# Kernel tuning notes

Measured on AMD Instinct MI355X. Metric: run time of the kernel, lower is better.

The kernel has to match this reference:

```python
import jax, jax.numpy as jnp
import numpy as np

B, N_PER, D = 128, 512, 128        # graphs, nodes per graph, feature width
N = B * N_PER                      # 65536 total nodes
E = 524288                         # total edges (avg degree 8)
KS = (410, 328, 263)               # ceil(0.8*512), ceil(0.8*410), ceil(0.8*328)


def setup_inputs() -> dict:
    key = jax.random.key(0)
    ks = jax.random.split(key, 20)
    p = lambda k, shape: jax.random.normal(k, shape, jnp.float32) * 0.05
    rng = np.random.default_rng(0)
    g = rng.integers(0, B, size=E)
    s = rng.integers(0, N_PER, size=E)
    t = rng.integers(0, N_PER, size=E)
    edge_index = jnp.asarray(np.stack([g * N_PER + s, g * N_PER + t]).astype(np.int32))
    inp = {
        'x': jax.random.normal(ks[0], (N, 1, D), jnp.float32),
        'edge_index': edge_index,
    }
    i = 1
    for l in (1, 2, 3):
        inp[f'conv{l}_wl'] = p(ks[i], (D, D)); i += 1   # SAGEConv lin_l (neighbors) weight
        inp[f'conv{l}_bl'] = p(ks[i], (D,));  i += 1   # SAGEConv lin_l bias
        inp[f'conv{l}_wr'] = p(ks[i], (D, D)); i += 1   # SAGEConv lin_r (root) weight
        inp[f'pool{l}_w'] = p(ks[i], (D,));   i += 1   # TopKPooling score vector
    inp['lin1_w'] = p(ks[13], (128, 256)); inp['lin1_b'] = p(ks[14], (128,))
    inp['lin2_w'] = p(ks[15], (64, 128));  inp['lin2_b'] = p(ks[16], (64,))
    inp['lin3_w'] = p(ks[17], (1, 64));    inp['lin3_b'] = p(ks[18], (1,))
    return inp


def _sage(x, node_mask, src, dst, wl, bl, wr):
    # SAGEConv, mean aggregation: lin_l(mean_{j->i} x_j) + lin_r(x_i)
    em = (node_mask[src] & node_mask[dst]).astype(x.dtype)   # [E] valid-edge mask
    msum = jax.ops.segment_sum(x[src] * em[:, None], dst, num_segments=N)
    deg = jax.ops.segment_sum(em, dst, num_segments=N)
    mean = msum / jnp.maximum(deg, 1.0)[:, None]
    return mean @ wl.T + bl + x @ wr.T


def _topk_pool(x, node_mask, w, k):
    # TopKPooling: score = x.w/||w||; keep top-k per graph; gate kept x by tanh(score)
    score = (x @ w) / (jnp.linalg.norm(w) + 1e-16)           # [N]
    score = jnp.where(node_mask, score, -jnp.inf)
    _, idx = jax.lax.top_k(score.reshape(B, N_PER), k)       # [B, k] within-graph ids
    nm = jnp.zeros((B, N_PER), bool).at[jnp.arange(B)[:, None], idx].set(True).reshape(-1)
    x = jnp.where(nm[:, None], x * jnp.tanh(score)[:, None], 0.0)
    return x, nm


def _readout(x, node_mask, k):
    # cat([global_max_pool, global_mean_pool]) over the k surviving nodes per graph
    xb = x.reshape(B, N_PER, -1)
    mb = node_mask.reshape(B, N_PER, 1)
    gmax = jnp.max(jnp.where(mb, xb, -jnp.inf), axis=1)
    gmean = jnp.sum(jnp.where(mb, xb, 0.0), axis=1) / k
    return jnp.concatenate([gmax, gmean], axis=1)            # [B, 2D]


def _forward(edge_index, x, conv1_wl, conv1_bl, conv1_wr, pool1_w,
             conv2_wl, conv2_bl, conv2_wr, pool2_w,
             conv3_wl, conv3_bl, conv3_wr, pool3_w,
             lin1_w, lin1_b, lin2_w, lin2_b, lin3_w, lin3_b):
    src, dst = edge_index[0], edge_index[1]
    h = x[:, 0, :]                                           # x.squeeze(1) -> [N, D]
    nm = jnp.ones((N,), bool)
    layers = ((conv1_wl, conv1_bl, conv1_wr, pool1_w),
              (conv2_wl, conv2_bl, conv2_wr, pool2_w),
              (conv3_wl, conv3_bl, conv3_wr, pool3_w))
    reads = []
    for (wl, bl, wr, pw), k in zip(layers, KS):
        h = jax.nn.relu(_sage(h, nm, src, dst, wl, bl, wr))
        h, nm = _topk_pool(h, nm, pw, k)
        reads.append(_readout(h, nm, float(k)))
    z = reads[0] + reads[1] + reads[2]                       # [B, 256]
    z = jax.nn.relu(z @ lin1_w.T + lin1_b)
    z = jax.nn.relu(z @ lin2_w.T + lin2_b)
    # dropout p=0.5 is a no-op at eval time
    return jax.nn.sigmoid(z @ lin3_w.T + lin3_b)[:, 0]       # [B]


def reference(x, edge_index, conv1_wl, conv1_bl, conv1_wr, pool1_w,
              conv2_wl, conv2_bl, conv2_wr, pool2_w,
              conv3_wl, conv3_bl, conv3_wr, pool3_w,
              lin1_w, lin1_b, lin2_w, lin2_b, lin3_w, lin3_b):
    return _forward(edge_index, x, conv1_wl, conv1_bl, conv1_wr, pool1_w,
                    conv2_wl, conv2_bl, conv2_wr, pool2_w,
                    conv3_wl, conv3_bl, conv3_wr, pool3_w,
                    lin1_w, lin1_b, lin2_w, lin2_b, lin3_w, lin3_b)
```

## Files before the change

### kernel.cpp

```cpp
#include <hip/hip_runtime.h>
#include <math.h>

#define NND 65536
#define NPER 512
#define NGR 128
#define DD 128
#define NED 524288

typedef __attribute__((ext_vector_type(8))) short short8;
typedef __attribute__((ext_vector_type(4))) float f32x4;

__device__ __forceinline__ unsigned short f2b(float f) {
  unsigned u = __float_as_uint(f);
  return (unsigned short)((u + 0x7FFFu + ((u >> 16) & 1u)) >> 16);
}
__device__ __forceinline__ float b2f(unsigned short h) {
  return __uint_as_float(((unsigned)h) << 16);
}


__global__ __launch_bounds__(256) void setup_kernel(
    int* __restrict__ counts, float2* __restrict__ tm,
    const float* __restrict__ wl0, const float* __restrict__ wr0,
    const float* __restrict__ wl1, const float* __restrict__ wr1,
    const float* __restrict__ wl2, const float* __restrict__ wr2,
    unsigned short* __restrict__ Whi, unsigned short* __restrict__ Wlo) {
  const int e = blockIdx.x * 256 + threadIdx.x;
  if (e < NND) {
    counts[e] = 0;
    tm[e] = make_float2(1.f, 1.f);
  }
  const float* wls[3] = {wl0, wl1, wl2};
  const float* wrs[3] = {wr0, wr1, wr2};
  int l = e >> 15;
  int o = e & 32767;
  int j = o & 7;
  int lane = (o >> 3) & 63;
  int nt = (o >> 9) & 7;
  int kc = o >> 12;
  int li = lane & 15, q = lane >> 4;
  int n = nt * 16 + li;
  int k = kc * 32 + q * 8 + j;
  const float* src = (k < 128) ? wls[l] : wrs[l];
  float v = src[n * DD + (k & 127)];
  unsigned short hi = f2b(v);
  Whi[e] = hi;
  Wlo[e] = f2b(v - b2f(hi));
}

__global__ __launch_bounds__(256) void hist_kernel(const int* __restrict__ ei,
                                                   int* __restrict__ counts) {
  int e = blockIdx.x * 256 + threadIdx.x;
  atomicAdd(&counts[ei[NED + e]], 1);
}

__global__ __launch_bounds__(1024) void scan_kernel(const int* __restrict__ counts,
                                                    int* __restrict__ off,
                                                    int* __restrict__ cursor) {
  __shared__ int part[1024];
  int t = threadIdx.x;
  int base = t * 64;
  int s = 0;
  const int4* c4 = (const int4*)(counts + base);
  for (int i = 0; i < 16; ++i) {
    int4 v = c4[i];
    s += v.x + v.y + v.z + v.w;
  }
  part[t] = s;
  __syncthreads();
  for (int d = 1; d < 1024; d <<= 1) {
    int v = (t >= d) ? part[t - d] : 0;
    __syncthreads();
    part[t] += v;
    __syncthreads();
  }
  int run = (t == 0) ? 0 : part[t - 1];
  for (int i = 0; i < 64; ++i) {
    off[base + i] = run;
    cursor[base + i] = run;
    run += counts[base + i];
  }
  if (t == 1023) off[NND] = NED;
}

__global__ __launch_bounds__(256) void scatter_kernel(const int* __restrict__ ei,
                                                      int* __restrict__ cursor,
                                                      int* __restrict__ ssrc) {
  int e = blockIdx.x * 256 + threadIdx.x;
  int dst = ei[NED + e];
  int pos = atomicAdd(&cursor[dst], 1);
  ssrc[pos] = ei[e];
}


template <int FIRST>
__device__ __forceinline__ void agg_group4(const int d0, const float* __restrict__ x,
                                           const float2* __restrict__ tm,
                                           const int* __restrict__ off,
                                           const int* __restrict__ ssrc,
                                           unsigned short* __restrict__ mhi,
                                           unsigned short* __restrict__ mlo,
                                           const int lane) {
  const int half = lane >> 5;
  const int l = lane & 31;
  int offv = 0;
  if (lane < 5) offv = off[d0 + lane];
  float deadv = 1.f;
  if (!FIRST && lane < 4) deadv = tm[d0 + lane].x;
  const int b0 = __shfl(offv, 0);
  const int b1 = __shfl(offv, 1);
  const int b2 = __shfl(offv, 2);
  const int b3 = __shfl(offv, 3);
  const int e3 = __shfl(offv, 4);
  float dds[4] = {1.f, 1.f, 1.f, 1.f};
  if (!FIRST) {
    dds[0] = __shfl(deadv, 0);
    dds[1] = __shfl(deadv, 1);
    dds[2] = __shfl(deadv, 2);
    dds[3] = __shfl(deadv, 3);
  }
  const int begs[4] = {b0, b1, b2, b3};
  const int ends[4] = {b1, b2, b3, e3};

  float4 acc[4];
  int deg[4];
#pragma unroll
  for (int d = 0; d < 4; ++d) {
    acc[d] = make_float4(0.f, 0.f, 0.f, 0.f);
    deg[d] = 0;
  }

  for (int base = b0; base < e3; base += 64) {
    const int nwin = min(64, e3 - base);
    int sv = 0;
    float tv = 0.f;
    int live = 0;
    if (lane < nwin) {
      sv = ssrc[base + lane];
      if (!FIRST) {
        const float2 mt = tm[sv];
        live = (mt.x != 0.f);
        tv = mt.y;
      }
    }
    unsigned long long bl;
    if (!FIRST)
      bl = __ballot(live);
    else
      bl = (nwin == 64) ? ~0ull : ((1ull << nwin) - 1);

#pragma unroll
    for (int d = 0; d < 4; ++d) {
      if (!FIRST && dds[d] == 0.f) continue;
      const int lo = max(begs[d], base);
      const int hi = min(ends[d], base + 64);
      if (lo >= hi) continue;
      const int j0 = lo - base;
      const int j1 = hi - base;
      const unsigned long long wm =
          (((j1 == 64) ? ~0ull : ((1ull << j1) - 1)) & ~((1ull << j0) - 1));
      deg[d] += (int)__popcll(bl & wm);
      int j = j0 + half;
      for (; j + 6 < j1; j += 8) {
        const int s0 = __shfl(sv, j);
        const int s1 = __shfl(sv, j + 2);
        const int s2 = __shfl(sv, j + 4);
        const int s3 = __shfl(sv, j + 6);
        const float4 v0 = *(const float4*)(x + (size_t)s0 * DD + l * 4);
        const float4 v1 = *(const float4*)(x + (size_t)s1 * DD + l * 4);
        const float4 v2 = *(const float4*)(x + (size_t)s2 * DD + l * 4);
        const float4 v3 = *(const float4*)(x + (size_t)s3 * DD + l * 4);
        if (!FIRST) {
          const float t0 = __shfl(tv, j), t1 = __shfl(tv, j + 2);
          const float t2 = __shfl(tv, j + 4), t3 = __shfl(tv, j + 6);
          acc[d].x += v0.x * t0 + v1.x * t1 + v2.x * t2 + v3.x * t3;
          acc[d].y += v0.y * t0 + v1.y * t1 + v2.y * t2 + v3.y * t3;
          acc[d].z += v0.z * t0 + v1.z * t1 + v2.z * t2 + v3.z * t3;
          acc[d].w += v0.w * t0 + v1.w * t1 + v2.w * t2 + v3.w * t3;
        } else {
          acc[d].x += v0.x + v1.x + v2.x + v3.x;
          acc[d].y += v0.y + v1.y + v2.y + v3.y;
          acc[d].z += v0.z + v1.z + v2.z + v3.z;
          acc[d].w += v0.w + v1.w + v2.w + v3.w;
        }
      }
      for (; j < j1; j += 2) {
        const int s = __shfl(sv, j);
        const float4 v = *(const float4*)(x + (size_t)s * DD + l * 4);
        if (!FIRST) {
          const float t = __shfl(tv, j);
          acc[d].x += v.x * t;
          acc[d].y += v.y * t;
          acc[d].z += v.z * t;
          acc[d].w += v.w * t;
        } else {
          acc[d].x += v.x;
          acc[d].y += v.y;
          acc[d].z += v.z;
          acc[d].w += v.w;
        }
      }
    }
  }

#pragma unroll
  for (int d = 0; d < 4; ++d) {
    float4 a = acc[d];
    a.x += __shfl(a.x, lane ^ 32);
    a.y += __shfl(a.y, lane ^ 32);
    a.z += __shfl(a.z, lane ^ 32);
    a.w += __shfl(a.w, lane ^ 32);
    if (lane < 32) {
      const float inv = (!FIRST && dds[d] == 0.f) ? 0.f : (1.f / (float)max(deg[d], 1));
      float4 m;
      m.x = a.x * inv;
      m.y = a.y * inv;
      m.z = a.z * inv;
      m.w = a.w * inv;
      ushort4 hv, lv;
      hv.x = f2b(m.x); lv.x = f2b(m.x - b2f(hv.x));
      hv.y = f2b(m.y); lv.y = f2b(m.y - b2f(hv.y));
      hv.z = f2b(m.z); lv.z = f2b(m.z - b2f(hv.z));
      hv.w = f2b(m.w); lv.w = f2b(m.w - b2f(hv.w));
      const size_t ad = (size_t)(d0 + d) * DD + l * 4;
      *(ushort4*)(mhi + ad) = hv;
      *(ushort4*)(mlo + ad) = lv;
    }
  }
}


#define GBM 64

struct GemmSmem {
  short Ah[2048];
  short Al[2048];
  float s_sp[4][GBM];
};

template <int FIRST>
__global__ __launch_bounds__(256) void aggemm_kernel_t(
    const float* __restrict__ x, const float2* __restrict__ tm,
    const int* __restrict__ off, const int* __restrict__ ssrc,
    unsigned short* __restrict__ mhi, unsigned short* __restrict__ mlo,
    const unsigned short* __restrict__ Whi, const unsigned short* __restrict__ Wlo,
    const float* __restrict__ bias, const float* __restrict__ pw,
    float* __restrict__ outp, float* __restrict__ sraw) {
  __shared__ GemmSmem sm;
  const int tid = threadIdx.x;
  const int wv = tid >> 6;
  const int lane = tid & 63;
  const int q = lane >> 4;
  const int li = lane & 15;
  const int bid = blockIdx.x;
  const int xcd = bid & 7;
  const int slot = bid >> 3;
  const int graph = xcd * 16 + (slot >> 3);
  const int mtile = slot & 7;
  const int row0 = graph * NPER + mtile * GBM;

#pragma unroll
  for (int s = 0; s < 4; ++s)
    agg_group4<FIRST>(row0 + (s * 4 + wv) * 4, x, tm, off, ssrc, mhi, mlo, lane);
  __syncthreads();

  int sdst[2];
  float ts[2];
#pragma unroll
  for (int i = 0; i < 2; ++i) {
    const int id = tid + i * 256;
    const int r = id >> 3;
    const int kb = (id & 7) << 2;
    sdst[i] = ((r >> 4) * 64 + (kb >> 3) * 16 + (r & 15)) * 8 + (kb & 7);
    ts[i] = FIRST ? 1.f : tm[row0 + r].y;
  }

  f32x4 acc[4][2];
#pragma unroll
  for (int m = 0; m < 4; ++m)
#pragma unroll
    for (int n = 0; n < 2; ++n) acc[m][n] = (f32x4){0.f, 0.f, 0.f, 0.f};

  float4 pa[2];
  ushort4 pmh[2], pml[2];
  short8 pbh[2], pbl[2];

#define LOADA(KC)                                                                      \
  {                                                                                    \
    if ((KC) < 4) {                                                                    \
      const int cb = (KC)*32;                                                          \
      _Pragma("unroll") for (int i = 0; i < 2; ++i) {                                  \
        const int id = tid + i * 256;                                                  \
        const size_t ga = (size_t)(row0 + (id >> 3)) * DD + cb + ((id & 7) << 2);      \
        pmh[i] = *(const ushort4*)(mhi + ga);                                          \
        pml[i] = *(const ushort4*)(mlo + ga);                                          \
      }                                                                                \
    } else {                                                                           \
      const int cb = ((KC)&3) * 32;                                                    \
      _Pragma("unroll") for (int i = 0; i < 2; ++i) {                                  \
        const int id = tid + i * 256;                                                  \
        pa[i] = *(const float4*)(x + (size_t)(row0 + (id >> 3)) * DD + cb + ((id & 7) << 2)); \
        if (!FIRST) {                                                                  \
          pa[i].x *= ts[i]; pa[i].y *= ts[i]; pa[i].z *= ts[i]; pa[i].w *= ts[i];      \
        }                                                                              \
      }                                                                                \
    }                                                                                  \
  }
#define LOADB(KC)                                                                      \
  {                                                                                    \
    _Pragma("unroll") for (int n = 0; n < 2; ++n) {                                    \
      const int ga = (((KC)*8 + wv * 2 + n) * 64 + lane) * 8;                          \
      pbh[n] = *(const short8*)(Whi + ga);                                             \
      pbl[n] = *(const short8*)(Wlo + ga);                                             \
    }                                                                                  \
  }

  LOADA(0) LOADB(0)

#pragma unroll
  for (int kc = 0; kc < 8; ++kc) {
    if (kc < 4) {
#pragma unroll
      for (int i = 0; i < 2; ++i) {
        *(ushort4*)(sm.Ah + sdst[i]) = pmh[i];
        *(ushort4*)(sm.Al + sdst[i]) = pml[i];
      }
    } else {
#pragma unroll
      for (int i = 0; i < 2; ++i) {
        ushort4 hv, lv;
        hv.x = f2b(pa[i].x); lv.x = f2b(pa[i].x - b2f(hv.x));
        hv.y = f2b(pa[i].y); lv.y = f2b(pa[i].y - b2f(hv.y));
        hv.z = f2b(pa[i].z); lv.z = f2b(pa[i].z - b2f(hv.z));
        hv.w = f2b(pa[i].w); lv.w = f2b(pa[i].w - b2f(hv.w));
        *(ushort4*)(sm.Ah + sdst[i]) = hv;
        *(ushort4*)(sm.Al + sdst[i]) = lv;
      }
    }
    short8 bh[2], bl[2];
    bh[0] = pbh[0]; bh[1] = pbh[1];
    bl[0] = pbl[0]; bl[1] = pbl[1];
    __syncthreads();
    short8 ah[4], al[4];
#pragma unroll
    for (int m = 0; m < 4; ++m) {
      ah[m] = *(const short8*)(sm.Ah + (m * 64 + lane) * 8);
      al[m] = *(const short8*)(sm.Al + (m * 64 + lane) * 8);
    }
    switch (kc) {
      case 0: LOADA(1) LOADB(1) break;
      case 1: LOADA(2) LOADB(2) break;
      case 2: LOADA(3) LOADB(3) break;
      case 3: LOADA(4) LOADB(4) break;
      case 4: LOADA(5) LOADB(5) break;
      case 5: LOADA(6) LOADB(6) break;
      case 6: LOADA(7) LOADB(7) break;
      default: break;
    }
#pragma unroll
    for (int m = 0; m < 4; ++m)
#pragma unroll
      for (int n = 0; n < 2; ++n) {
        acc[m][n] = __builtin_amdgcn_mfma_f32_16x16x32_bf16(ah[m], bh[n], acc[m][n], 0, 0, 0);
        acc[m][n] = __builtin_amdgcn_mfma_f32_16x16x32_bf16(ah[m], bl[n], acc[m][n], 0, 0, 0);
        acc[m][n] = __builtin_amdgcn_mfma_f32_16x16x32_bf16(al[m], bh[n], acc[m][n], 0, 0, 0);
      }
    __syncthreads();
  }
#undef LOADA
#undef LOADB

  const int c0 = wv * 32 + li;
  const int c1 = wv * 32 + 16 + li;
  const float b0 = bias[c0], b1 = bias[c1];
  const float p0 = pw[c0], p1 = pw[c1];
  float sp[16];
#pragma unroll
  for (int m = 0; m < 4; ++m) {
#pragma unroll
    for (int i = 0; i < 4; ++i) {
      const int r = row0 + m * 16 + q * 4 + i;
      const float v0 = fmaxf(acc[m][0][i] + b0, 0.f);
      const float v1 = fmaxf(acc[m][1][i] + b1, 0.f);
      outp[(size_t)r * DD + c0] = v0;
      outp[(size_t)r * DD + c1] = v1;
      sp[m * 4 + i] = v0 * p0 + v1 * p1;
    }
  }
#pragma unroll
  for (int e = 0; e < 16; ++e) {
    sp[e] += __shfl_xor(sp[e], 1);
    sp[e] += __shfl_xor(sp[e], 2);
    sp[e] += __shfl_xor(sp[e], 4);
    sp[e] += __shfl_xor(sp[e], 8);
  }
  if (li == 0) {
#pragma unroll
    for (int e = 0; e < 16; ++e) sm.s_sp[wv][(e >> 2) * 16 + q * 4 + (e & 3)] = sp[e];
  }
  __syncthreads();
  if (tid < GBM)
    sraw[row0 + tid] = sm.s_sp[0][tid] + sm.s_sp[1][tid] + sm.s_sp[2][tid] + sm.s_sp[3][tid];
}


__global__ __launch_bounds__(256) void pool_kernel(const float* __restrict__ h,
                                                   const float* __restrict__ sraw,
                                                   const float* __restrict__ pw,
                                                   const float2* __restrict__ tmP,
                                                   float2* __restrict__ tmN,
                                                   float* __restrict__ zp,
                                                   const int kk) {
  __shared__ float s_sc[NPER];
  __shared__ float s_t[128];
  __shared__ unsigned char s_sel[128];
  __shared__ int s_rk[256];
  __shared__ float4 red4[512];
  __shared__ float s_norm;
  const int b = blockIdx.x;
  const int g = b >> 2;
  const int q = b & 3;
  const int tid = threadIdx.x;
  const int lane = tid & 63;

  if (tid < 64) {
    const float v0 = pw[lane], v1 = pw[lane + 64];
    float p = v0 * v0 + v1 * v1;
#pragma unroll
    for (int o = 32; o > 0; o >>= 1) p += __shfl_down(p, o);
    if (lane == 0) s_norm = 1.f / (sqrtf(p) + 1e-16f);
  }
  __syncthreads();
  const float inv_norm = s_norm;
#pragma unroll
  for (int i = 0; i < 2; ++i) {
    const int n = tid + i * 256;
    const int node = g * NPER + n;
    s_sc[n] = (tmP[node].x != 0.f) ? sraw[node] * inv_norm : -INFINITY;
  }
  __syncthreads();

  {
    const int n = q * 128 + (tid & 127);
    const int jb = (tid >> 7) * 256;
    const float s = s_sc[n];
    int rank = 0;
    for (int j = jb; j < jb + 256; ++j) {
      const float sj = s_sc[j];
      rank += (sj > s || (sj == s && j < n)) ? 1 : 0;
    }
    s_rk[tid] = rank;
  }
  __syncthreads();
  if (tid < 128) {
    const int n = q * 128 + tid;
    const int rank = s_rk[tid] + s_rk[tid + 128];
    const int sel = (rank < kk) ? 1 : 0;
    const float s = s_sc[n];
    const float t = sel ? tanhf(s) : 0.f;
    tmN[g * NPER + n] = make_float2(sel ? 1.f : 0.f, t);
    s_sel[tid] = (unsigned char)sel;
    s_t[tid] = t;
  }
  __syncthreads();

  const int c = tid & 31;
  const int r = tid >> 5;
  float4 pmax = make_float4(-INFINITY, -INFINITY, -INFINITY, -INFINITY);
  float4 psum = make_float4(0.f, 0.f, 0.f, 0.f);
  const size_t nbase = (size_t)g * NPER + q * 128;
  const float4* h4 = (const float4*)h;
  for (int i = 0; i < 16; ++i) {
    const int nl = r + 8 * i;
    if (s_sel[nl]) {
      float4 v = h4[(nbase + nl) * 32 + c];
      const float t = s_t[nl];
      v.x *= t; v.y *= t; v.z *= t; v.w *= t;
      pmax.x = fmaxf(pmax.x, v.x);
      pmax.y = fmaxf(pmax.y, v.y);
      pmax.z = fmaxf(pmax.z, v.z);
      pmax.w = fmaxf(pmax.w, v.w);
      psum.x += v.x; psum.y += v.y; psum.z += v.z; psum.w += v.w;
    }
  }
  red4[r * 32 + c] = pmax;
  red4[256 + r * 32 + c] = psum;
  __syncthreads();
  if (tid < 32) {
    float4 m = red4[tid];
    float4 sm2 = red4[256 + tid];
#pragma unroll
    for (int rr = 1; rr < 8; ++rr) {
      const float4 a = red4[rr * 32 + tid];
      const float4 s3 = red4[256 + rr * 32 + tid];
      m.x = fmaxf(m.x, a.x); m.y = fmaxf(m.y, a.y);
      m.z = fmaxf(m.z, a.z); m.w = fmaxf(m.w, a.w);
      sm2.x += s3.x; sm2.y += s3.y; sm2.z += s3.z; sm2.w += s3.w;
    }
    *(float4*)(zp + (size_t)b * 256 + tid * 4) = m;
    *(float4*)(zp + (size_t)b * 256 + 128 + tid * 4) = sm2;
  }
}


__global__ __launch_bounds__(128) void mlp_kernel(const float* __restrict__ zpart,
                                                  const float* __restrict__ w1,
                                                  const float* __restrict__ b1,
                                                  const float* __restrict__ w2,
                                                  const float* __restrict__ b2,
                                                  const float* __restrict__ w3,
                                                  const float* __restrict__ b3,
                                                  float* __restrict__ out) {
  __shared__ float z[256];
  __shared__ float h1[128];
  __shared__ float h2[64];
  const int g = blockIdx.x;
  const int t = threadIdx.x;
  const float iks[3] = {1.f / 410.f, 1.f / 328.f, 1.f / 263.f};
  float zmax = 0.f, zmean = 0.f;
#pragma unroll
  for (int l = 0; l < 3; ++l) {
    const float* zp = zpart + ((size_t)l * 512 + g * 4) * 256;
    zmax += fmaxf(fmaxf(zp[t], zp[256 + t]), fmaxf(zp[512 + t], zp[768 + t]));
    zmean += (zp[128 + t] + zp[384 + t] + zp[640 + t] + zp[896 + t]) * iks[l];
  }
  z[t] = zmax;
  z[128 + t] = zmean;
  __syncthreads();
  float a = b1[t];
  for (int k = 0; k < 256; ++k) a = fmaf(z[k], w1[t * 256 + k], a);
  h1[t] = fmaxf(a, 0.f);
  __syncthreads();
  if (t < 64) {
    float a2 = b2[t];
    for (int k = 0; k < 128; ++k) a2 = fmaf(h1[k], w2[t * 128 + k], a2);
    h2[t] = fmaxf(a2, 0.f);
  }
  __syncthreads();
  if (t == 0) {
    float a3 = b3[0];
    for (int k = 0; k < 64; ++k) a3 = fmaf(h2[k], w3[k], a3);
    out[g] = 1.f / (1.f + expf(-a3));
  }
}


extern "C" void kernel_launch(void* const* d_in, const int* in_sizes, int n_in,
                              void* d_out, int out_size, void* d_ws, size_t ws_size,
                              hipStream_t stream) {
  (void)in_sizes; (void)n_in; (void)out_size; (void)ws_size;
  const float* x_in = (const float*)d_in[0];
  const int* ei = (const int*)d_in[1];
  const float* wl[3] = {(const float*)d_in[2], (const float*)d_in[6], (const float*)d_in[10]};
  const float* cbl[3] = {(const float*)d_in[3], (const float*)d_in[7], (const float*)d_in[11]};
  const float* wr[3] = {(const float*)d_in[4], (const float*)d_in[8], (const float*)d_in[12]};
  const float* pw[3] = {(const float*)d_in[5], (const float*)d_in[9], (const float*)d_in[13]};
  const float* l1w = (const float*)d_in[14];
  const float* l1b = (const float*)d_in[15];
  const float* l2w = (const float*)d_in[16];
  const float* l2b = (const float*)d_in[17];
  const float* l3w = (const float*)d_in[18];
  const float* l3b = (const float*)d_in[19];
  float* out = (float*)d_out;

  char* w = (char*)d_ws;
  int* counts = (int*)(w + 0 * (1 << 20));
  int* off = (int*)(w + 1 * (1 << 20));
  int* cursor = (int*)(w + 2 * (1 << 20));
  float* sraw = (float*)(w + 2 * (1 << 20));
  float2* tmA = (float2*)(w + 3 * (1 << 20));
  float2* tmB = (float2*)(w + 3 * (1 << 20) + (1 << 19));
  float* zpart = (float*)(w + 4 * (1 << 20));
  unsigned short* Whi = (unsigned short*)(w + 5 * (1 << 20) + (1 << 19));
  unsigned short* Wlo = (unsigned short*)(w + 5 * (1 << 20) + 3 * (1 << 18));
  int* ssrc = (int*)(w + 6 * (1 << 20));
  unsigned short* mhi = (unsigned short*)(w + (size_t)8 * (1 << 20));
  unsigned short* mlo = (unsigned short*)(w + (size_t)24 * (1 << 20));
  float* hA = (float*)(w + (size_t)40 * (1 << 20));
  float* hB = (float*)(w + (size_t)72 * (1 << 20));

  setup_kernel<<<384, 256, 0, stream>>>(counts, tmA, wl[0], wr[0], wl[1], wr[1], wl[2], wr[2],
                                        Whi, Wlo);
  hist_kernel<<<NED / 256, 256, 0, stream>>>(ei, counts);
  scan_kernel<<<1, 1024, 0, stream>>>(counts, off, cursor);
  scatter_kernel<<<NED / 256, 256, 0, stream>>>(ei, cursor, ssrc);

  const int ks[3] = {410, 328, 263};
  const float* xl = x_in;
  float* houts[3] = {hA, hB, hA};
  float2* tprev[3] = {tmA, tmB, tmA};
  float2* tnext[3] = {tmB, tmA, tmB};
  for (int l = 0; l < 3; ++l) {
    float* hout = houts[l];
    if (l == 0)
      aggemm_kernel_t<1><<<1024, 256, 0, stream>>>(xl, tprev[l], off, ssrc, mhi, mlo,
                                                   Whi + (size_t)l * 32768,
                                                   Wlo + (size_t)l * 32768, cbl[l], pw[l],
                                                   hout, sraw);
    else
      aggemm_kernel_t<0><<<1024, 256, 0, stream>>>(xl, tprev[l], off, ssrc, mhi, mlo,
                                                   Whi + (size_t)l * 32768,
                                                   Wlo + (size_t)l * 32768, cbl[l], pw[l],
                                                   hout, sraw);
    pool_kernel<<<NGR * 4, 256, 0, stream>>>(hout, sraw, pw[l], tprev[l], tnext[l],
                                             zpart + (size_t)l * 512 * 256, ks[l]);
    xl = hout;
  }
  mlp_kernel<<<NGR, 128, 0, stream>>>(zpart, l1w, l1b, l2w, l2b, l3w, l3b, out);
}
```

Before: 425.2 us.

## Fuse top-k pooling and readout into next layer's aggregation-GEMM kernel

Removes the separate pool kernels: each layer kernel recomputes the previous layer's per-graph top-k selection (rank by counting over 512 scores in shared memory), gate values and partial readout, then runs aggregation and GEMM. Aggregated means go directly into an LDS tile in MFMA layout instead of a global bf16 staging buffer, and the M-tile is halved to 32 rows with 2048 blocks. The last pooling and readout move into the MLP kernel. The cost is redundant rank computation in every block of a graph (16x) and a smaller GEMM tile with no software pipelining.

Measured after the change: 525.7 us. 1.24x slower.

```diff
diff --git a/kernel.cpp b/kernel.cpp
--- a/kernel.cpp
+++ b/kernel.cpp
@@ -20,16 +20,13 @@
 
 
 __global__ __launch_bounds__(256) void setup_kernel(
-    int* __restrict__ counts, float2* __restrict__ tm,
+    int* __restrict__ counts,
     const float* __restrict__ wl0, const float* __restrict__ wr0,
     const float* __restrict__ wl1, const float* __restrict__ wr1,
     const float* __restrict__ wl2, const float* __restrict__ wr2,
     unsigned short* __restrict__ Whi, unsigned short* __restrict__ Wlo) {
   const int e = blockIdx.x * 256 + threadIdx.x;
-  if (e < NND) {
-    counts[e] = 0;
-    tm[e] = make_float2(1.f, 1.f);
-  }
+  if (e < NND) counts[e] = 0;
   const float* wls[3] = {wl0, wl1, wl2};
   const float* wrs[3] = {wr0, wr1, wr2};
   int l = e >> 15;
@@ -93,20 +90,33 @@
 }
 
 
+__device__ __forceinline__ int rank_of(const float* s_sc, const float s, const int n) {
+  int r = 0;
+  for (int j = 0; j < NPER; j += 4) {
+    const float4 sj = *(const float4*)(s_sc + j);
+    r += (sj.x > s || (sj.x == s && (j + 0) < n)) ? 1 : 0;
+    r += (sj.y > s || (sj.y == s && (j + 1) < n)) ? 1 : 0;
+    r += (sj.z > s || (sj.z == s && (j + 2) < n)) ? 1 : 0;
+    r += (sj.w > s || (sj.w == s && (j + 3) < n)) ? 1 : 0;
+  }
+  return r;
+}
+
+
 template <int FIRST>
-__device__ __forceinline__ void agg_group4(const int d0, const float* __restrict__ x,
-                                           const float2* __restrict__ tm,
+__device__ __forceinline__ void agg_group4(const int gi, const int row0, const int gl0,
+                                           const float* __restrict__ x,
+                                           const float2* s_tm,
                                            const int* __restrict__ off,
                                            const int* __restrict__ ssrc,
-                                           unsigned short* __restrict__ mhi,
-                                           unsigned short* __restrict__ mlo,
-                                           const int lane) {
+                                           short* Mh, short* Ml, const int lane) {
   const int half = lane >> 5;
   const int l = lane & 31;
+  const int d0 = row0 + gi * 4;
   int offv = 0;
   if (lane < 5) offv = off[d0 + lane];
   float deadv = 1.f;
-  if (!FIRST && lane < 4) deadv = tm[d0 + lane].x;
+  if (!FIRST && lane < 4) deadv = s_tm[gl0 + gi * 4 + lane].x;
   const int b0 = __shfl(offv, 0);
   const int b1 = __shfl(offv, 1);
   const int b2 = __shfl(offv, 2);
@@ -138,7 +148,7 @@
     if (lane < nwin) {
       sv = ssrc[base + lane];
       if (!FIRST) {
-        const float2 mt = tm[sv];
+        const float2 mt = s_tm[sv & (NPER - 1)];
         live = (mt.x != 0.f);
         tv = mt.y;
       }
@@ -152,11 +162,11 @@
 #pragma unroll
     for (int d = 0; d < 4; ++d) {
       if (!FIRST && dds[d] == 0.f) continue;
-      const int lo = max(begs[d], base);
-      const int hi = min(ends[d], base + 64);
-      if (lo >= hi) continue;
-      const int j0 = lo - base;
-      const int j1 = hi - base;
+      const int wlo = max(begs[d], base);
+      const int whi = min(ends[d], base + 64);
+      if (wlo >= whi) continue;
+      const int j0 = wlo - base;
+      const int j1 = whi - base;
       const unsigned long long wm =
           (((j1 == 64) ? ~0ull : ((1ull << j1) - 1)) & ~((1ull << j0) - 1));
       deg[d] += (int)__popcll(bl & wm);
@@ -217,36 +227,40 @@
       m.y = a.y * inv;
       m.z = a.z * inv;
       m.w = a.w * inv;
+      const int rloc = gi * 4 + d;
+      const int mm = rloc >> 4;
+      const int ri = rloc & 15;
+      const int kc2 = l >> 3;
+      const int q2 = (l & 7) >> 1;
+      const int h4 = l & 1;
+      const int idx = ((kc2 * 2 + mm) * 64 + q2 * 16 + ri) * 8 + h4 * 4;
       ushort4 hv, lv;
       hv.x = f2b(m.x); lv.x = f2b(m.x - b2f(hv.x));
       hv.y = f2b(m.y); lv.y = f2b(m.y - b2f(hv.y));
       hv.z = f2b(m.z); lv.z = f2b(m.z - b2f(hv.z));
       hv.w = f2b(m.w); lv.w = f2b(m.w - b2f(hv.w));
-      const size_t ad = (size_t)(d0 + d) * DD + l * 4;
-      *(ushort4*)(mhi + ad) = hv;
-      *(ushort4*)(mlo + ad) = lv;
-    }
-  }
-}
-
-
-#define GBM 64
-
-struct GemmSmem {
-  short Ah[2048];
-  short Al[2048];
-  float s_sp[4][GBM];
-};
-
-template <int FIRST>
-__global__ __launch_bounds__(256) void aggemm_kernel_t(
-    const float* __restrict__ x, const float2* __restrict__ tm,
+      *(ushort4*)(Mh + idx) = hv;
+      *(ushort4*)(Ml + idx) = lv;
+    }
+  }
+}
+
+
+template <int L>
+__global__ __launch_bounds__(256) void layer_kernel(
+    const float* __restrict__ x, const float* __restrict__ sprev,
+    const float2* __restrict__ tmPrev, const float* __restrict__ pwPrev,
+    const int kkPrev, float2* __restrict__ tmOut, float* __restrict__ zpOut,
     const int* __restrict__ off, const int* __restrict__ ssrc,
-    unsigned short* __restrict__ mhi, unsigned short* __restrict__ mlo,
     const unsigned short* __restrict__ Whi, const unsigned short* __restrict__ Wlo,
     const float* __restrict__ bias, const float* __restrict__ pw,
     float* __restrict__ outp, float* __restrict__ sraw) {
-  __shared__ GemmSmem sm;
+  __shared__ short Mh[4096];
+  __shared__ short Ml[4096];
+  __shared__ float2 s_tm[NPER];
+  __shared__ alignas(16) float scbuf[1024];
+  __shared__ float s_sp[4][32];
+  __shared__ float s_norm;
   const int tid = threadIdx.x;
   const int wv = tid >> 6;
   const int lane = tid & 63;
@@ -255,128 +269,165 @@
   const int bid = blockIdx.x;
   const int xcd = bid & 7;
   const int slot = bid >> 3;
-  const int graph = xcd * 16 + (slot >> 3);
-  const int mtile = slot & 7;
-  const int row0 = graph * NPER + mtile * GBM;
-
-#pragma unroll
-  for (int s = 0; s < 4; ++s)
-    agg_group4<FIRST>(row0 + (s * 4 + wv) * 4, x, tm, off, ssrc, mhi, mlo, lane);
-  __syncthreads();
-
-  int sdst[2];
-  float ts[2];
-#pragma unroll
-  for (int i = 0; i < 2; ++i) {
-    const int id = tid + i * 256;
-    const int r = id >> 3;
-    const int kb = (id & 7) << 2;
-    sdst[i] = ((r >> 4) * 64 + (kb >> 3) * 16 + (r & 15)) * 8 + (kb & 7);
-    ts[i] = FIRST ? 1.f : tm[row0 + r].y;
-  }
-
-  f32x4 acc[4][2];
-#pragma unroll
-  for (int m = 0; m < 4; ++m)
+  const int graph = xcd * 16 + (slot >> 4);
+  const int mtile = slot & 15;
+  const int row0 = graph * NPER + mtile * 32;
+  const int gl0 = mtile * 32;
+
+  if (L > 0) {
+    if (tid < 64) {
+      const float v0 = pwPrev[lane], v1 = pwPrev[lane + 64];
+      float p = v0 * v0 + v1 * v1;
+#pragma unroll
+      for (int o = 32; o > 0; o >>= 1) p += __shfl_down(p, o);
+      if (lane == 0) s_norm = 1.f / (sqrtf(p) + 1e-16f);
+    }
+    __syncthreads();
+    const float inv_norm = s_norm;
+    const int node0 = graph * NPER + tid;
+    const int node1 = node0 + 256;
+    float sc0 = sprev[node0] * inv_norm;
+    float sc1 = sprev[node1] * inv_norm;
+    if (L == 2) {
+      if (tmPrev[node0].x == 0.f) sc0 = -INFINITY;
+      if (tmPrev[node1].x == 0.f) sc1 = -INFINITY;
+    }
+    scbuf[tid] = sc0;
+    scbuf[tid + 256] = sc1;
+    __syncthreads();
+    const int r0 = rank_of(scbuf, sc0, tid);
+    const int r1 = rank_of(scbuf, sc1, tid + 256);
+    const float2 tm0 = (r0 < kkPrev) ? make_float2(1.f, tanhf(sc0)) : make_float2(0.f, 0.f);
+    const float2 tm1 = (r1 < kkPrev) ? make_float2(1.f, tanhf(sc1)) : make_float2(0.f, 0.f);
+    s_tm[tid] = tm0;
+    s_tm[tid + 256] = tm1;
+    if (mtile == 0) {
+      tmOut[node0] = tm0;
+      tmOut[node1] = tm1;
+    }
+    __syncthreads();
+
+    {
+      float4* red4 = (float4*)scbuf;
+      const int c = tid & 31;
+      const int rg = tid >> 5;
+      float4 rmax = make_float4(-INFINITY, -INFINITY, -INFINITY, -INFINITY);
+      float4 rsum = make_float4(0.f, 0.f, 0.f, 0.f);
+#pragma unroll
+      for (int i = 0; i < 4; ++i) {
+        const int rloc = rg + 8 * i;
+        const float2 mt = s_tm[gl0 + rloc];
+        float4 v = *(const float4*)(x + (size_t)(row0 + rloc) * DD + c * 4);
+        v.x *= mt.y; v.y *= mt.y; v.z *= mt.y; v.w *= mt.y;
+        rsum.x += v.x; rsum.y += v.y; rsum.z += v.z; rsum.w += v.w;
+        if (mt.x != 0.f) {
+          rmax.x = fmaxf(rmax.x, v.x);
+          rmax.y = fmaxf(rmax.y, v.y);
+          rmax.z = fmaxf(rmax.z, v.z);
+          rmax.w = fmaxf(rmax.w, v.w);
+        }
+      }
+      red4[rg * 32 + c] = rmax;
+      __syncthreads();
+      float4 zm = make_float4(0.f, 0.f, 0.f, 0.f);
+      if (tid < 32) {
+        zm = red4[tid];
+#pragma unroll
+        for (int rr = 1; rr < 8; ++rr) {
+          const float4 a = red4[rr * 32 + tid];
+          zm.x = fmaxf(zm.x, a.x); zm.y = fmaxf(zm.y, a.y);
+          zm.z = fmaxf(zm.z, a.z); zm.w = fmaxf(zm.w, a.w);
+        }
+      }
+      __syncthreads();
+      red4[rg * 32 + c] = rsum;
+      __syncthreads();
+      if (tid < 32) {
+        float4 zs = red4[tid];
+#pragma unroll
+        for (int rr = 1; rr < 8; ++rr) {
+          const float4 a = red4[rr * 32 + tid];
+          zs.x += a.x; zs.y += a.y; zs.z += a.z; zs.w += a.w;
+        }
+        float* zp = zpOut + (size_t)(graph * 16 + mtile) * 256;
+        *(float4*)(zp + tid * 4) = zm;
+        *(float4*)(zp + 128 + tid * 4) = zs;
+      }
+    }
+  }
+
+#pragma unroll
+  for (int s = 0; s < 2; ++s)
+    agg_group4<(L == 0)>(s * 4 + wv, row0, gl0, x, s_tm, off, ssrc, Mh, Ml, lane);
+  __syncthreads();
+
+  float tsm[2] = {1.f, 1.f};
+  if (L > 0) {
+    tsm[0] = s_tm[gl0 + li].y;
+    tsm[1] = s_tm[gl0 + 16 + li].y;
+  }
+  f32x4 acc[2][2];
+#pragma unroll
+  for (int m = 0; m < 2; ++m)
 #pragma unroll
     for (int n = 0; n < 2; ++n) acc[m][n] = (f32x4){0.f, 0.f, 0.f, 0.f};
 
-  float4 pa[2];
-  ushort4 pmh[2], pml[2];
-  short8 pbh[2], pbl[2];
-
-#define LOADA(KC)                                                                      \
-  {                                                                                    \
-    if ((KC) < 4) {                                                                    \
-      const int cb = (KC)*32;                                                          \
-      _Pragma("unroll") for (int i = 0; i < 2; ++i) {                                  \
-        const int id = tid + i * 256;                                                  \
-        const size_t ga = (size_t)(row0 + (id >> 3)) * DD + cb + ((id & 7) << 2);      \
-        pmh[i] = *(const ushort4*)(mhi + ga);                                          \
-        pml[i] = *(const ushort4*)(mlo + ga);                                          \
-      }                                                                                \
-    } else {                                                                           \
-      const int cb = ((KC)&3) * 32;                                                    \
-      _Pragma("unroll") for (int i = 0; i < 2; ++i) {                                  \
-        const int id = tid + i * 256;                                                  \
-        pa[i] = *(const float4*)(x + (size_t)(row0 + (id >> 3)) * DD + cb + ((id & 7) << 2)); \
-        if (!FIRST) {                                                                  \
-          pa[i].x *= ts[i]; pa[i].y *= ts[i]; pa[i].z *= ts[i]; pa[i].w *= ts[i];      \
-        }                                                                              \
-      }                                                                                \
-    }                                                                                  \
-  }
-#define LOADB(KC)                                                                      \
-  {                                                                                    \
-    _Pragma("unroll") for (int n = 0; n < 2; ++n) {                                    \
-      const int ga = (((KC)*8 + wv * 2 + n) * 64 + lane) * 8;                          \
-      pbh[n] = *(const short8*)(Whi + ga);                                             \
-      pbl[n] = *(const short8*)(Wlo + ga);                                             \
-    }                                                                                  \
-  }
-
-  LOADA(0) LOADB(0)
-
 #pragma unroll
   for (int kc = 0; kc < 8; ++kc) {
+    short8 ah[2], al[2], bh[2], bl[2];
     if (kc < 4) {
 #pragma unroll
-      for (int i = 0; i < 2; ++i) {
-        *(ushort4*)(sm.Ah + sdst[i]) = pmh[i];
-        *(ushort4*)(sm.Al + sdst[i]) = pml[i];
+      for (int m = 0; m < 2; ++m) {
+        const int idx = ((kc * 2 + m) * 64 + lane) * 8;
+        ah[m] = *(const short8*)(Mh + idx);
+        al[m] = *(const short8*)(Ml + idx);
       }
     } else {
 #pragma unroll
-      for (int i = 0; i < 2; ++i) {
-        ushort4 hv, lv;
-        hv.x = f2b(pa[i].x); lv.x = f2b(pa[i].x - b2f(hv.x));
-        hv.y = f2b(pa[i].y); lv.y = f2b(pa[i].y - b2f(hv.y));
-        hv.z = f2b(pa[i].z); lv.z = f2b(pa[i].z - b2f(hv.z));
-        hv.w = f2b(pa[i].w); lv.w = f2b(pa[i].w - b2f(hv.w));
-        *(ushort4*)(sm.Ah + sdst[i]) = hv;
-        *(ushort4*)(sm.Al + sdst[i]) = lv;
-      }
-    }
-    short8 bh[2], bl[2];
-    bh[0] = pbh[0]; bh[1] = pbh[1];
-    bl[0] = pbl[0]; bl[1] = pbl[1];
-    __syncthreads();
-    short8 ah[4], al[4];
-#pragma unroll
-    for (int m = 0; m < 4; ++m) {
-      ah[m] = *(const short8*)(sm.Ah + (m * 64 + lane) * 8);
-      al[m] = *(const short8*)(sm.Al + (m * 64 + lane) * 8);
-    }
-    switch (kc) {
-      case 0: LOADA(1) LOADB(1) break;
-      case 1: LOADA(2) LOADB(2) break;
-      case 2: LOADA(3) LOADB(3) break;
-      case 3: LOADA(4) LOADB(4) break;
-      case 4: LOADA(5) LOADB(5) break;
-      case 5: LOADA(6) LOADB(6) break;
-      case 6: LOADA(7) LOADB(7) break;
-      default: break;
-    }
-#pragma unroll
-    for (int m = 0; m < 4; ++m)
+      for (int m = 0; m < 2; ++m) {
+        const float* xr = x + (size_t)(row0 + m * 16 + li) * DD + (kc - 4) * 32 + q * 8;
+        float4 f0 = *(const float4*)xr;
+        float4 f1 = *(const float4*)(xr + 4);
+        if (L > 0) {
+          const float t = tsm[m];
+          f0.x *= t; f0.y *= t; f0.z *= t; f0.w *= t;
+          f1.x *= t; f1.y *= t; f1.z *= t; f1.w *= t;
+        }
+        const float fv[8] = {f0.x, f0.y, f0.z, f0.w, f1.x, f1.y, f1.z, f1.w};
+        short8 hh, ll;
+#pragma unroll
+        for (int e = 0; e < 8; ++e) {
+          const unsigned short h = f2b(fv[e]);
+          hh[e] = (short)h;
+          ll[e] = (short)f2b(fv[e] - b2f(h));
+        }
+        ah[m] = hh;
+        al[m] = ll;
+      }
+    }
+#pragma unroll
+    for (int n = 0; n < 2; ++n) {
+      const int ga = ((kc * 8 + wv * 2 + n) * 64 + lane) * 8;
+      bh[n] = *(const short8*)(Whi + ga);
+      bl[n] = *(const short8*)(Wlo + ga);
+    }
+#pragma unroll
+    for (int m = 0; m < 2; ++m)
 #pragma unroll
       for (int n = 0; n < 2; ++n) {
         acc[m][n] = __builtin_amdgcn_mfma_f32_16x16x32_bf16(ah[m], bh[n], acc[m][n], 0, 0, 0);
         acc[m][n] = __builtin_amdgcn_mfma_f32_16x16x32_bf16(ah[m], bl[n], acc[m][n], 0, 0, 0);
         acc[m][n] = __builtin_amdgcn_mfma_f32_16x16x32_bf16(al[m], bh[n], acc[m][n], 0, 0, 0);
       }
-    __syncthreads();
-  }
-#undef LOADA
-#undef LOADB
+  }
 
   const int c0 = wv * 32 + li;
-  const int c1 = wv * 32 + 16 + li;
+  const int c1 = c0 + 16;
   const float b0 = bias[c0], b1 = bias[c1];
   const float p0 = pw[c0], p1 = pw[c1];
-  float sp[16];
-#pragma unroll
-  for (int m = 0; m < 4; ++m) {
+  float sp[8];
+#pragma unroll
+  for (int m = 0; m < 2; ++m) {
 #pragma unroll
     for (int i = 0; i < 4; ++i) {
       const int r = row0 + m * 16 + q * 4 + i;
@@ -388,7 +439,7 @@
     }
   }
 #pragma unroll
-  for (int e = 0; e < 16; ++e) {
+  for (int e = 0; e < 8; ++e) {
     sp[e] += __shfl_xor(sp[e], 1);
     sp[e] += __shfl_xor(sp[e], 2);
     sp[e] += __shfl_xor(sp[e], 4);
@@ -396,35 +447,33 @@
   }
   if (li == 0) {
 #pragma unroll
-    for (int e = 0; e < 16; ++e) sm.s_sp[wv][(e >> 2) * 16 + q * 4 + (e & 3)] = sp[e];
-  }
-  __syncthreads();
-  if (tid < GBM)
-    sraw[row0 + tid] = sm.s_sp[0][tid] + sm.s_sp[1][tid] + sm.s_sp[2][tid] + sm.s_sp[3][tid];
-}
-
-
-__global__ __launch_bounds__(256) void pool_kernel(const float* __restrict__ h,
-                                                   const float* __restrict__ sraw,
-                                                   const float* __restrict__ pw,
-                                                   const float2* __restrict__ tmP,
-                                                   float2* __restrict__ tmN,
-                                                   float* __restrict__ zp,
-                                                   const int kk) {
-  __shared__ float s_sc[NPER];
-  __shared__ float s_t[128];
-  __shared__ unsigned char s_sel[128];
-  __shared__ int s_rk[256];
-  __shared__ float4 red4[512];
+    for (int e = 0; e < 8; ++e) s_sp[wv][(e >> 2) * 16 + q * 4 + (e & 3)] = sp[e];
+  }
+  __syncthreads();
+  if (tid < 32)
+    sraw[row0 + tid] = s_sp[0][tid] + s_sp[1][tid] + s_sp[2][tid] + s_sp[3][tid];
+}
+
+
+__global__ __launch_bounds__(256) void mlp_kernel(
+    const float* __restrict__ h3, const float* __restrict__ s2buf,
+    const float2* __restrict__ tm2, const float* __restrict__ pw2,
+    const float* __restrict__ zpart,
+    const float* __restrict__ w1, const float* __restrict__ b1,
+    const float* __restrict__ w2, const float* __restrict__ b2,
+    const float* __restrict__ w3, const float* __restrict__ b3,
+    float* __restrict__ out) {
+  __shared__ float2 s_tm[NPER];
+  __shared__ alignas(16) float scbuf[1024];
+  __shared__ float z3m[128], z3s[128];
+  __shared__ float z[256], sh1[128], sh2[64];
   __shared__ float s_norm;
-  const int b = blockIdx.x;
-  const int g = b >> 2;
-  const int q = b & 3;
+  const int g = blockIdx.x;
   const int tid = threadIdx.x;
   const int lane = tid & 63;
 
   if (tid < 64) {
-    const float v0 = pw[lane], v1 = pw[lane + 64];
+    const float v0 = pw2[lane], v1 = pw2[lane + 64];
     float p = v0 * v0 + v1 * v1;
 #pragma unroll
     for (int o = 32; o > 0; o >>= 1) p += __shfl_down(p, o);
@@ -432,114 +481,95 @@
   }
   __syncthreads();
   const float inv_norm = s_norm;
-#pragma unroll
-  for (int i = 0; i < 2; ++i) {
-    const int n = tid + i * 256;
-    const int node = g * NPER + n;
-    s_sc[n] = (tmP[node].x != 0.f) ? sraw[node] * inv_norm : -INFINITY;
-  }
+  const int node0 = g * NPER + tid;
+  const int node1 = node0 + 256;
+  float sc0 = (tm2[node0].x != 0.f) ? s2buf[node0] * inv_norm : -INFINITY;
+  float sc1 = (tm2[node1].x != 0.f) ? s2buf[node1] * inv_norm : -INFINITY;
+  scbuf[tid] = sc0;
+  scbuf[tid + 256] = sc1;
+  __syncthreads();
+  const int r0 = rank_of(scbuf, sc0, tid);
+  const int r1 = rank_of(scbuf, sc1, tid + 256);
+  s_tm[tid] = (r0 < 263) ? make_float2(1.f, tanhf(sc0)) : make_float2(0.f, 0.f);
+  s_tm[tid + 256] = (r1 < 263) ? make_float2(1.f, tanhf(sc1)) : make_float2(0.f, 0.f);
   __syncthreads();
 
   {
-    const int n = q * 128 + (tid & 127);
-    const int jb = (tid >> 7) * 256;
-    const float s = s_sc[n];
-    int rank = 0;
-    for (int j = jb; j < jb + 256; ++j) {
-      const float sj = s_sc[j];
-      rank += (sj > s || (sj == s && j < n)) ? 1 : 0;
-    }
-    s_rk[tid] = rank;
-  }
-  __syncthreads();
+    float4* red4 = (float4*)scbuf;
+    const int c = tid & 31;
+    const int rg = tid >> 5;
+    float4 rmax = make_float4(-INFINITY, -INFINITY, -INFINITY, -INFINITY);
+    float4 rsum = make_float4(0.f, 0.f, 0.f, 0.f);
+    for (int i = 0; i < 64; ++i) {
+      const int rloc = rg + 8 * i;
+      const float2 mt = s_tm[rloc];
+      float4 v = *(const float4*)(h3 + (size_t)(g * NPER + rloc) * DD + c * 4);
+      v.x *= mt.y; v.y *= mt.y; v.z *= mt.y; v.w *= mt.y;
+      rsum.x += v.x; rsum.y += v.y; rsum.z += v.z; rsum.w += v.w;
+      if (mt.x != 0.f) {
+        rmax.x = fmaxf(rmax.x, v.x);
+        rmax.y = fmaxf(rmax.y, v.y);
+        rmax.z = fmaxf(rmax.z, v.z);
+        rmax.w = fmaxf(rmax.w, v.w);
+      }
+    }
+    red4[rg * 32 + c] = rmax;
+    __syncthreads();
+    float4 zm = make_float4(0.f, 0.f, 0.f, 0.f);
+    if (tid < 32) {
+      zm = red4[tid];
+#pragma unroll
+      for (int rr = 1; rr < 8; ++rr) {
+        const float4 a = red4[rr * 32 + tid];
+        zm.x = fmaxf(zm.x, a.x); zm.y = fmaxf(zm.y, a.y);
+        zm.z = fmaxf(zm.z, a.z); zm.w = fmaxf(zm.w, a.w);
+      }
+    }
+    __syncthreads();
+    red4[rg * 32 + c] = rsum;
+    __syncthreads();
+    if (tid < 32) {
+      float4 zs = red4[tid];
+#pragma unroll
+      for (int rr = 1; rr < 8; ++rr) {
+        const float4 a = red4[rr * 32 + tid];
+        zs.x += a.x; zs.y += a.y; zs.z += a.z; zs.w += a.w;
+      }
+      *(float4*)(z3m + tid * 4) = zm;
+      *(float4*)(z3s + tid * 4) = zs;
+    }
+  }
+  __syncthreads();
+
   if (tid < 128) {
-    const int n = q * 128 + tid;
-    const int rank = s_rk[tid] + s_rk[tid + 128];
-    const int sel = (rank < kk) ? 1 : 0;
-    const float s = s_sc[n];
-    const float t = sel ? tanhf(s) : 0.f;
-    tmN[g * NPER + n] = make_float2(sel ? 1.f : 0.f, t);
-    s_sel[tid] = (unsigned char)sel;
-    s_t[tid] = t;
-  }
-  __syncthreads();
-
-  const int c = tid & 31;
-  const int r = tid >> 5;
-  float4 pmax = make_float4(-INFINITY, -INFINITY, -INFINITY, -INFINITY);
-  float4 psum = make_float4(0.f, 0.f, 0.f, 0.f);
-  const size_t nbase = (size_t)g * NPER + q * 128;
-  const float4* h4 = (const float4*)h;
-  for (int i = 0; i < 16; ++i) {
-    const int nl = r + 8 * i;
-    if (s_sel[nl]) {
-      float4 v = h4[(nbase + nl) * 32 + c];
-      const float t = s_t[nl];
-      v.x *= t; v.y *= t; v.z *= t; v.w *= t;
-      pmax.x = fmaxf(pmax.x, v.x);
-      pmax.y = fmaxf(pmax.y, v.y);
-      pmax.z = fmaxf(pmax.z, v.z);
-      pmax.w = fmaxf(pmax.w, v.w);
-      psum.x += v.x; psum.y += v.y; psum.z += v.z; psum.w += v.w;
-    }
-  }
-  red4[r * 32 + c] = pmax;
-  red4[256 + r * 32 + c] = psum;
-  __syncthreads();
-  if (tid < 32) {
-    float4 m = red4[tid];
-    float4 sm2 = red4[256 + tid];
-#pragma unroll
-    for (int rr = 1; rr < 8; ++rr) {
-      const float4 a = red4[rr * 32 + tid];
-      const float4 s3 = red4[256 + rr * 32 + tid];
-      m.x = fmaxf(m.x, a.x); m.y = fmaxf(m.y, a.y);
-      m.z = fmaxf(m.z, a.z); m.w = fmaxf(m.w, a.w);
-      sm2.x += s3.x; sm2.y += s3.y; sm2.z += s3.z; sm2.w += s3.w;
-    }
-    *(float4*)(zp + (size_t)b * 256 + tid * 4) = m;
-    *(float4*)(zp + (size_t)b * 256 + 128 + tid * 4) = sm2;
-  }
-}
-
-
-__global__ __launch_bounds__(128) void mlp_kernel(const float* __restrict__ zpart,
-                                                  const float* __restrict__ w1,
-                                                  const float* __restrict__ b1,
-                                                  const float* __restrict__ w2,
-                                                  const float* __restrict__ b2,
-                                                  const float* __restrict__ w3,
-                                                  const float* __restrict__ b3,
-                                                  float* __restrict__ out) {
-  __shared__ float z[256];
-  __shared__ float h1[128];
-  __shared__ float h2[64];
-  const int g = blockIdx.x;
-  const int t = threadIdx.x;
-  const float iks[3] = {1.f / 410.f, 1.f / 328.f, 1.f / 263.f};
-  float zmax = 0.f, zmean = 0.f;
-#pragma unroll
-  for (int l = 0; l < 3; ++l) {
-    const float* zp = zpart + ((size_t)l * 512 + g * 4) * 256;
-    zmax += fmaxf(fmaxf(zp[t], zp[256 + t]), fmaxf(zp[512 + t], zp[768 + t]));
-    zmean += (zp[128 + t] + zp[384 + t] + zp[640 + t] + zp[896 + t]) * iks[l];
-  }
-  z[t] = zmax;
-  z[128 + t] = zmean;
-  __syncthreads();
-  float a = b1[t];
-  for (int k = 0; k < 256; ++k) a = fmaf(z[k], w1[t * 256 + k], a);
-  h1[t] = fmaxf(a, 0.f);
-  __syncthreads();
-  if (t < 64) {
-    float a2 = b2[t];
-    for (int k = 0; k < 128; ++k) a2 = fmaf(h1[k], w2[t * 128 + k], a2);
-    h2[t] = fmaxf(a2, 0.f);
-  }
-  __syncthreads();
-  if (t == 0) {
+    float m0 = -INFINITY, s0 = 0.f, m1 = -INFINITY, s1 = 0.f;
+    for (int t = 0; t < 16; ++t) {
+      const float* zp0 = zpart + (size_t)(g * 16 + t) * 256;
+      const float* zp1 = zpart + (size_t)2048 * 256 + (size_t)(g * 16 + t) * 256;
+      m0 = fmaxf(m0, zp0[tid]);
+      s0 += zp0[128 + tid];
+      m1 = fmaxf(m1, zp1[tid]);
+      s1 += zp1[128 + tid];
+    }
+    z[tid] = m0 + m1 + z3m[tid];
+    z[128 + tid] = s0 * (1.f / 410.f) + s1 * (1.f / 328.f) + z3s[tid] * (1.f / 263.f);
+  }
+  __syncthreads();
+  if (tid < 128) {
+    float a = b1[tid];
+    for (int k = 0; k < 256; ++k) a = fmaf(z[k], w1[tid * 256 + k], a);
+    sh1[tid] = fmaxf(a, 0.f);
+  }
+  __syncthreads();
+  if (tid < 64) {
+    float a2 = b2[tid];
+    for (int k = 0; k < 128; ++k) a2 = fmaf(sh1[k], w2[tid * 128 + k], a2);
+    sh2[tid] = fmaxf(a2, 0.f);
+  }
+  __syncthreads();
+  if (tid == 0) {
     float a3 = b3[0];
-    for (int k = 0; k < 64; ++k) a3 = fmaf(h2[k], w3[k], a3);
+    for (int k = 0; k < 64; ++k) a3 = fmaf(sh2[k], w3[k], a3);
     out[g] = 1.f / (1.f + expf(-a3));
   }
 }
@@ -567,44 +597,33 @@
   int* counts = (int*)(w + 0 * (1 << 20));
   int* off = (int*)(w + 1 * (1 << 20));
   int* cursor = (int*)(w + 2 * (1 << 20));
-  float* sraw = (float*)(w + 2 * (1 << 20));
-  float2* tmA = (float2*)(w + 3 * (1 << 20));
-  float2* tmB = (float2*)(w + 3 * (1 << 20) + (1 << 19));
-  float* zpart = (float*)(w + 4 * (1 << 20));
-  unsigned short* Whi = (unsigned short*)(w + 5 * (1 << 20) + (1 << 19));
-  unsigned short* Wlo = (unsigned short*)(w + 5 * (1 << 20) + 3 * (1 << 18));
-  int* ssrc = (int*)(w + 6 * (1 << 20));
-  unsigned short* mhi = (unsigned short*)(w + (size_t)8 * (1 << 20));
-  unsigned short* mlo = (unsigned short*)(w + (size_t)24 * (1 << 20));
-  float* hA = (float*)(w + (size_t)40 * (1 << 20));
-  float* hB = (float*)(w + (size_t)72 * (1 << 20));
-
-  setup_kernel<<<384, 256, 0, stream>>>(counts, tmA, wl[0], wr[0], wl[1], wr[1], wl[2], wr[2],
+  int* ssrc = (int*)(w + 3 * (1 << 20));
+  unsigned short* Whi = (unsigned short*)(w + 5 * (1 << 20) + (1 << 18));
+  unsigned short* Wlo = (unsigned short*)(w + 5 * (1 << 20) + (1 << 19));
+  float* s0 = (float*)(w + 6 * (1 << 20));
+  float* s1 = (float*)(w + 6 * (1 << 20) + (1 << 18));
+  float* s2 = (float*)(w + 6 * (1 << 20) + (1 << 19));
+  float2* tmA = (float2*)(w + 7 * (1 << 20));
+  float2* tmB = (float2*)(w + 7 * (1 << 20) + (1 << 19));
+  float* zpart = (float*)(w + 8 * (1 << 20));
+  float* hA = (float*)(w + (size_t)16 * (1 << 20));
+  float* hB = (float*)(w + (size_t)48 * (1 << 20));
+
+  setup_kernel<<<384, 256, 0, stream>>>(counts, wl[0], wr[0], wl[1], wr[1], wl[2], wr[2],
                                         Whi, Wlo);
   hist_kernel<<<NED / 256, 256, 0, stream>>>(ei, counts);
   scan_kernel<<<1, 1024, 0, stream>>>(counts, off, cursor);
   scatter_kernel<<<NED / 256, 256, 0, stream>>>(ei, cursor, ssrc);
 
-  const int ks[3] = {410, 328, 263};
-  const float* xl = x_in;
-  float* houts[3] = {hA, hB, hA};
-  float2* tprev[3] = {tmA, tmB, tmA};
-  float2* tnext[3] = {tmB, tmA, tmB};
-  for (int l = 0; l < 3; ++l) {
-    float* hout = houts[l];
-    if (l == 0)
-      aggemm_kernel_t<1><<<1024, 256, 0, stream>>>(xl, tprev[l], off, ssrc, mhi, mlo,
-                                                   Whi + (size_t)l * 32768,
-                                                   Wlo + (size_t)l * 32768, cbl[l], pw[l],
-                                                   hout, sraw);
-    else
-      aggemm_kernel_t<0><<<1024, 256, 0, stream>>>(xl, tprev[l], off, ssrc, mhi, mlo,
-                                                   Whi + (size_t)l * 32768,
-                                                   Wlo + (size_t)l * 32768, cbl[l], pw[l],
-                                                   hout, sraw);
-    pool_kernel<<<NGR * 4, 256, 0, stream>>>(hout, sraw, pw[l], tprev[l], tnext[l],
-                                             zpart + (size_t)l * 512 * 256, ks[l]);
-    xl = hout;
-  }
-  mlp_kernel<<<NGR, 128, 0, stream>>>(zpart, l1w, l1b, l2w, l2b, l3w, l3b, out);
-}
+  layer_kernel<0><<<2048, 256, 0, stream>>>(x_in, nullptr, nullptr, nullptr, 0, nullptr,
+                                            nullptr, off, ssrc, Whi, Wlo, cbl[0], pw[0],
+                                            hA, s0);
+  layer_kernel<1><<<2048, 256, 0, stream>>>(hA, s0, nullptr, pw[0], 410, tmA, zpart, off,
+                                            ssrc, Whi + 32768, Wlo + 32768, cbl[1], pw[1],
+                                            hB, s1);
+  layer_kernel<2><<<2048, 256, 0, stream>>>(hB, s1, tmA, pw[1], 328, tmB,
+                                            zpart + (size_t)2048 * 256, off, ssrc,
+                                            Whi + 65536, Wlo + 65536, cbl[2], pw[2], hA, s2);
+  mlp_kernel<<<NGR, 256, 0, stream>>>(hA, s2, tmB, pw[2], zpart, l1w, l1b, l2w, l2b, l3w,
+                                      l3b, out);
+}
```
